# Optimization experiments

Measured on AMD Instinct MI355X. Metric: run time of the kernel, lower is better.

The kernel has to match this reference:

```python
import jax, jax.numpy as jnp
import numpy as np

POOL = 2  # maxout pool size


def setup_inputs() -> dict:
    key = jax.random.key(0)
    ks = jax.random.split(key, 20)
    V, WV, ENC, DEC, ATT = 32000, 512, 512, 512, 512
    T, B, S, L = 32, 64, 256, 1
    IN = WV + ENC  # input_feed: emb concat context
    sc = 0.02
    emb_table = jax.random.normal(ks[0], (V, WV), jnp.float32) * sc
    emb_table = emb_table.at[0].set(0.0)  # padding_idx = PAD = 0
    inp = {
        'input_ids': jax.random.randint(ks[1], (T, B), 0, V),
        'hidden': jax.random.normal(ks[2], (L, B, DEC), jnp.float32),
        'context': jax.random.normal(ks[3], (S, B, ENC), jnp.float32),
        'src_pad_mask': jnp.zeros((B, S), jnp.float32),
        'init_att': jax.random.normal(ks[4], (B, ENC), jnp.float32),
        'emb_table': emb_table,
        'W_ih': jax.random.normal(ks[5], (3 * DEC, IN), jnp.float32) * sc,
        'W_hh': jax.random.normal(ks[6], (3 * DEC, DEC), jnp.float32) * sc,
        'b_ih': jnp.zeros((3 * DEC,), jnp.float32),
        'b_hh': jnp.zeros((3 * DEC,), jnp.float32),
        'W_pre': jax.random.normal(ks[7], (ATT, ENC), jnp.float32) * sc,
        'b_pre': jnp.zeros((ATT,), jnp.float32),
        'W_q': jax.random.normal(ks[8], (ATT, DEC), jnp.float32) * sc,
        'v_att': jax.random.normal(ks[9], (ATT,), jnp.float32) * sc,
        'W_copy': jax.random.normal(ks[10], (1, ENC + DEC), jnp.float32) * sc,
        'b_copy': jnp.zeros((1,), jnp.float32),
        'W_read': jax.random.normal(ks[11], (DEC, ENC + DEC + WV), jnp.float32) * sc,
        'b_read': jnp.zeros((DEC,), jnp.float32),
    }
    return inp


def reference(input_ids, hidden, context, src_pad_mask, init_att, emb_table,
              W_ih, W_hh, b_ih, b_hh, W_pre, b_pre, W_q, v_att,
              W_copy, b_copy, W_read, b_read):
    T, B = input_ids.shape
    dec = hidden.shape[-1]
    ctx_t = jnp.transpose(context, (1, 0, 2))            # [B, S, enc]
    # ConcatAttention precompute (done once, reused each step)
    precompute = jnp.einsum('bse,ae->bsa', ctx_t, W_pre) + b_pre  # [B, S, att]
    emb = emb_table[input_ids]                           # [T, B, wv]

    def gru_cell(x, h):
        gx = x @ W_ih.T + b_ih
        gh = h @ W_hh.T + b_hh
        xr, xz, xn = jnp.split(gx, 3, axis=-1)
        hr, hz, hn = jnp.split(gh, 3, axis=-1)
        r = jax.nn.sigmoid(xr + hr)
        z = jax.nn.sigmoid(xz + hz)
        n = jnp.tanh(xn + r * hn)
        return (1.0 - z) * n + z * h

    def step(carry, emb_t):
        h, cur_ctx = carry                               # h: [1,B,dec]
        x = jnp.concatenate([emb_t, cur_ctx], axis=1)    # input_feed
        h_new = gru_cell(x, h[0])
        out = h_new                                      # single layer output
        # concat attention
        target = out @ W_q.T                             # [B, att]
        tmp = jnp.tanh(precompute + target[:, None, :])  # [B, S, att]
        energy = jnp.einsum('bsa,a->bs', tmp, v_att)
        energy = energy * (1.0 - src_pad_mask) + src_pad_mask * (-1e6)
        score = jax.nn.softmax(energy, axis=-1)          # [B, S]
        new_ctx = jnp.einsum('bs,bse->be', score, ctx_t)
        # copy gate
        copy_p = jax.nn.sigmoid(
            jnp.concatenate([out, new_ctx], axis=1) @ W_copy.T + b_copy)
        # readout + maxout (dropout is identity at eval)
        readout = jnp.concatenate([emb_t, out, new_ctx], axis=1) @ W_read.T + b_read
        mo = readout.reshape(B, dec // POOL, POOL).max(axis=-1)
        return (h_new[None], new_ctx), (mo, score, copy_p)

    (hid, cur_ctx), (g_out, c_out, copy_out) = jax.lax.scan(
        step, (hidden, init_att), emb)
    return g_out, c_out, copy_out, hid, c_out[-1], cur_ctx
```

## Files before the change

kernel.cpp:

```cpp
#include <hip/hip_runtime.h>
#include <hip/hip_bf16.h>


typedef unsigned int uint;
typedef unsigned short ushort;
typedef __attribute__((ext_vector_type(8))) short s8v;
typedef __attribute__((ext_vector_type(4))) float f4v;

#define DD 512

__device__ __forceinline__ float sigmf(float x) { return 1.0f / (1.0f + __expf(-x)); }
__device__ __forceinline__ float tanh_fast(float x) {
    float e = __expf(2.0f * x);
    return 1.0f - 2.0f / (e + 1.0f);
}
__device__ __forceinline__ ushort f2bf(float f) {
    uint b = __float_as_uint(f);
    return (ushort)((b + 0x7FFFu + ((b >> 16) & 1u)) >> 16);
}
__device__ __forceinline__ uint pk2(float a, float b) {
    return (uint)f2bf(a) | ((uint)f2bf(b) << 16);
}
__device__ __forceinline__ float bfl(uint u) { return __uint_as_float(u << 16); }
__device__ __forceinline__ float bfh(uint u) { return __uint_as_float(u & 0xFFFF0000u); }
__device__ __forceinline__ f4v MFMA(s8v a, s8v b, f4v c) {
    return __builtin_amdgcn_mfma_f32_16x16x32_bf16(a, b, c, 0, 0, 0);
}

__device__ __forceinline__ void gbar(uint* c, uint target) {
    __syncthreads();
    if (threadIdx.x == 0) {
        asm volatile("s_waitcnt vmcnt(0) lgkmcnt(0)" ::: "memory");
        __hip_atomic_fetch_add(c, 1u, __ATOMIC_RELAXED, __HIP_MEMORY_SCOPE_AGENT);
        while (__hip_atomic_load(c, __ATOMIC_RELAXED, __HIP_MEMORY_SCOPE_AGENT) < target)
            __builtin_amdgcn_s_sleep(1);
    }
    __syncthreads();
}

template <int MODE>
__global__ __launch_bounds__(256) void mgemm(
    const float* __restrict__ A0, const float* __restrict__ A1,
    const float* __restrict__ A2, const int* __restrict__ ids,
    const float* __restrict__ Bm, const float* __restrict__ bias,
    void* __restrict__ Cout, int ldb, int K)
{
    __shared__ __align__(16) ushort Ab[64 * 32];
    __shared__ __align__(16) ushort Bb[64 * 32];
    __shared__ int rid[64];
    const int tid = threadIdx.x;
    const int m0 = blockIdx.x * 64, n0 = blockIdx.y * 64;
    if (MODE != 0 && tid < 64) rid[tid] = ids[m0 + tid];
    const int lane = tid & 63;
    const int w = tid >> 6;
    const int srow = tid >> 2, sc = tid & 3;
    f4v acc[4];
#pragma unroll
    for (int mt = 0; mt < 4; ++mt) acc[mt] = (f4v){0.f, 0.f, 0.f, 0.f};

    for (int k0 = 0; k0 < K; k0 += 32) {
        __syncthreads();
        {
            const float* ap;
            int m = m0 + srow;
            if (MODE == 0) {
                ap = A0 + (size_t)(m & 255) * 32768 + (size_t)(m >> 8) * 512 + k0 + sc * 8;
            } else if (MODE == 1) {
                ap = A0 + (size_t)rid[srow] * 512 + k0 + sc * 8;
            } else {
                if (k0 < 512)       ap = A0 + (size_t)rid[srow] * 512 + k0 + sc * 8;
                else if (k0 < 1024) ap = A1 + (size_t)m * 512 + (k0 - 512) + sc * 8;
                else                ap = A2 + (size_t)m * 512 + (k0 - 1024) + sc * 8;
            }
            float4 v0 = *(const float4*)ap;
            float4 v1 = *(const float4*)(ap + 4);
            uint4 pa;
            pa.x = pk2(v0.x, v0.y); pa.y = pk2(v0.z, v0.w);
            pa.z = pk2(v1.x, v1.y); pa.w = pk2(v1.z, v1.w);
            *(uint4*)&Ab[srow * 32 + ((sc ^ (srow & 3)) << 3)] = pa;
            const float* bp = Bm + (size_t)(n0 + srow) * ldb + k0 + sc * 8;
            float4 w0 = *(const float4*)bp;
            float4 w1 = *(const float4*)(bp + 4);
            uint4 pb;
            pb.x = pk2(w0.x, w0.y); pb.y = pk2(w0.z, w0.w);
            pb.z = pk2(w1.x, w1.y); pb.w = pk2(w1.z, w1.w);
            *(uint4*)&Bb[srow * 32 + ((sc ^ (srow & 3)) << 3)] = pb;
        }
        __syncthreads();
        int rr = lane & 15, kc = lane >> 4;
        s8v bf = *(const s8v*)&Bb[(w * 16 + rr) * 32 + ((kc ^ (rr & 3)) << 3)];
#pragma unroll
        for (int mt = 0; mt < 4; ++mt) {
            s8v af = *(const s8v*)&Ab[(mt * 16 + rr) * 32 + ((kc ^ (rr & 3)) << 3)];
            acc[mt] = MFMA(af, bf, acc[mt]);
        }
    }
    float bv = bias[n0 + w * 16 + (lane & 15)];
#pragma unroll
    for (int mt = 0; mt < 4; ++mt) {
#pragma unroll
        for (int r2 = 0; r2 < 4; ++r2) {
            int m = m0 + mt * 16 + (lane >> 4) * 4 + r2;
            int n = n0 + w * 16 + (lane & 15);
            float v = acc[mt][r2] + bv;
            if (MODE == 0) {
                ((ushort*)Cout)[(size_t)m * 512 + n] = f2bf(v);
            } else if (MODE == 1) {
                ((float*)Cout)[(size_t)m * 1536 + n] = v;
            } else {
                float vm = fmaxf(v, __shfl_xor(v, 1));
                if (!(lane & 1)) ((float*)Cout)[(size_t)m * 256 + (n >> 1)] = vm;
            }
        }
    }
}

__global__ __launch_bounds__(512) void wprep2(
    const float* __restrict__ W_ih, const float* __restrict__ W_hh,
    const float* __restrict__ W_q,
    uint* __restrict__ Wpk, uint* __restrict__ WqT)
{
    int id = blockIdx.x * 512 + threadIdx.x;
    if (id < 786432) {
        int l4 = id & 255;
        int chunk = id >> 8;
        int g = chunk % 3;
        int t2 = chunk / 3;
        int ks = t2 & 15;
        int mat = (t2 >> 4) & 1;
        int u = t2 >> 5;
        int lane = l4 >> 2, e2 = l4 & 3;
        int n = g * 512 + u * 16 + (lane & 15);
        int k = ks * 32 + ((lane >> 4) << 3) + e2 * 2;
        float w0, w1;
        if (mat == 0) {
            w0 = W_ih[(size_t)n * 1024 + 512 + k];
            w1 = W_ih[(size_t)n * 1024 + 512 + k + 1];
        } else {
            w0 = W_hh[(size_t)n * 512 + k];
            w1 = W_hh[(size_t)n * 512 + k + 1];
        }
        Wpk[id] = pk2(w0, w1);
    } else if (id < 917504) {
        int rid2 = id - 786432;
        int kp = rid2 >> 9, a = rid2 & 511;
        WqT[rid2] = pk2(W_q[(size_t)a * 512 + 2 * kp], W_q[(size_t)a * 512 + 2 * kp + 1]);
    }
}

__global__ __launch_bounds__(512, 1) void k_steps(
    const float* __restrict__ gxe, const float* __restrict__ hidden,
    const float* __restrict__ init_att, const float* __restrict__ context,
    const float* __restrict__ mask, const float* __restrict__ v_att,
    const float* __restrict__ b_hh, const ushort* __restrict__ preb,
    const uint* __restrict__ Wpk, const uint* __restrict__ WqT,
    float* __restrict__ h_hist, float* __restrict__ ctx_hist,
    float* __restrict__ pe_buf, uint* __restrict__ cnt,
    float* __restrict__ cout)
{
    __shared__ __align__(16) ushort preT[256 * 128];
    __shared__ __align__(16) ushort ctxT[256 * 128];
    __shared__ __align__(16) float scr[6144];
    __shared__ float smask[256];
    __shared__ float svatt[128];

    const int tid = threadIdx.x;
    const int blk = blockIdx.x;
    const int q = blk >> 6;
    const int b = blk & 63;
    const int r = b & 7;
    const int u = ((b >> 3) << 2) | q;
    const int lane = tid & 63;
    const int wid = __builtin_amdgcn_readfirstlane(tid >> 6);

    uint* cl_cnt = cnt + b * 32;
    uint* gr_cnt = cnt + 2048 + r * 32;

#pragma unroll
    for (int cc = 0; cc < 8; ++cc) {
        int cid = tid * 8 + cc;
        int s = cid >> 4, ch = cid & 15;
        int sw = (s ^ (s >> 3)) & 7;
        uint4 pv = *(const uint4*)(preb + ((size_t)(b * 256 + s)) * 512 + q * 128 + ch * 8);
        *(uint4*)&preT[s * 128 + ((ch ^ sw) << 3)] = pv;
        const float* cp = context + ((size_t)s * 64 + b) * 512 + q * 128 + ch * 8;
        float4 c0 = *(const float4*)cp;
        float4 c1 = *(const float4*)(cp + 4);
        uint4 cv;
        cv.x = pk2(c0.x, c0.y); cv.y = pk2(c0.z, c0.w);
        cv.z = pk2(c1.x, c1.y); cv.w = pk2(c1.z, c1.w);
        *(uint4*)&ctxT[s * 128 + ch * 8] = cv;
    }
    if (tid < 256) smask[tid] = mask[b * 256 + tid];
    else if (tid < 384) svatt[tid - 256] = v_att[q * 128 + (tid - 256)];

    const int mat_w = wid >> 2, kw = wid & 3;
    s8v wr0[4], wr1[4], wr2[4];
#pragma unroll
    for (int s = 0; s < 4; ++s) {
        int ks = kw * 4 + s;
        const uint* wb = Wpk + ((((u * 2 + mat_w) * 16 + ks) * 3) << 8) + (lane << 2);
        wr0[s] = *(const s8v*)(wb);
        wr1[s] = *(const s8v*)(wb + 256);
        wr2[s] = *(const s8v*)(wb + 512);
    }
    const int a_p2 = tid & 127, dq_p2 = tid >> 7;
    uint wqreg[64];
#pragma unroll
    for (int i = 0; i < 64; ++i)
        wqreg[i] = WqT[(size_t)(dq_p2 * 64 + i) * 512 + q * 128 + a_p2];

    const int bloc = tid >> 4, jj = tid & 15;
    int bb_c = 0, d_c = 0, eidx = 0;
    float bh0 = 0.f, bh1 = 0.f, bh2 = 0.f;
    if (tid < 128) {
        bb_c = r + bloc * 8;
        d_c = u * 16 + jj;
        eidx = ((jj + ((bloc >> 2) << 4)) << 2) + (bloc & 3);
        bh0 = b_hh[d_c]; bh1 = b_hh[512 + d_c]; bh2 = b_hh[1024 + d_c];
    }

    for (int t = 0; t < 32; ++t) {
        const float* ctxp = t ? (ctx_hist + (size_t)(t - 1) * 32768) : init_att;
        const float* hp = t ? (h_hist + (size_t)(t - 1) * 32768) : hidden;

        float gx0 = 0.f, gx1 = 0.f, gx2 = 0.f, hpv = 0.f;
        if (tid < 128) {
            const float* gp = gxe + ((size_t)t * 64 + bb_c) * 1536 + d_c;
            gx0 = gp[0]; gx1 = gp[512]; gx2 = gp[1024];
            hpv = hp[(size_t)bb_c * 512 + d_c];
        }

        __syncthreads();
        {
            int c2 = tid & 31, row = (tid >> 5) & 7, mat = tid >> 8;
            const float* src = mat ? hp : ctxp;
            int bb = r + row * 8;
            const float* sp = src + (size_t)bb * 512 + c2 * 16;
            float4 v0 = *(const float4*)sp, v1 = *(const float4*)(sp + 4);
            float4 v2 = *(const float4*)(sp + 8), v3 = *(const float4*)(sp + 12);
            uint4 p0, p1;
            p0.x = pk2(v0.x, v0.y); p0.y = pk2(v0.z, v0.w);
            p0.z = pk2(v1.x, v1.y); p0.w = pk2(v1.z, v1.w);
            p1.x = pk2(v2.x, v2.y); p1.y = pk2(v2.z, v2.w);
            p1.z = pk2(v3.x, v3.y); p1.w = pk2(v3.z, v3.w);
            char* xb = (char*)scr + mat * 8192 + row * 1024;
            int c0 = c2 * 2;
            *(uint4*)(xb + ((c0 ^ row) << 4)) = p0;
            *(uint4*)(xb + (((c0 + 1) ^ row) << 4)) = p1;
        }
        __syncthreads();
        f4v ac0 = (f4v){0.f, 0.f, 0.f, 0.f};
        f4v ac1 = ac0, ac2 = ac0;
        {
            const char* xbase = (const char*)scr + mat_w * 8192 + (lane & 15) * 1024;
            int rsw = (lane & 15) & 7;
#pragma unroll
            for (int s = 0; s < 4; ++s) {
                int ch = kw * 16 + s * 4 + (lane >> 4);
                s8v af = *(const s8v*)(xbase + ((ch ^ rsw) << 4));
                ac0 = MFMA(af, wr0[s], ac0);
                ac1 = MFMA(af, wr1[s], ac1);
                ac2 = MFMA(af, wr2[s], ac2);
            }
        }
        __syncthreads();
        {
            f4v* rb = (f4v*)scr;
            rb[((mat_w * 3 + 0) * 4 + kw) * 64 + lane] = ac0;
            rb[((mat_w * 3 + 1) * 4 + kw) * 64 + lane] = ac1;
            rb[((mat_w * 3 + 2) * 4 + kw) * 64 + lane] = ac2;
        }
        __syncthreads();
        if (tid < 128) {
            float AX[3], AH[3];
#pragma unroll
            for (int g = 0; g < 3; ++g) {
                float sx = 0.f, sh = 0.f;
#pragma unroll
                for (int kw2 = 0; kw2 < 4; ++kw2) {
                    sx += scr[((0 + g) * 4 + kw2) * 256 + eidx];
                    sh += scr[((3 + g) * 4 + kw2) * 256 + eidx];
                }
                AX[g] = sx;
                AH[g] = sh;
            }
            AX[0] += gx0; AX[1] += gx1; AX[2] += gx2;
            AH[0] += bh0; AH[1] += bh1; AH[2] += bh2;
            float rr = sigmf(AX[0] + AH[0]);
            float zz = sigmf(AX[1] + AH[1]);
            float nn = tanh_fast(AX[2] + rr * AH[2]);
            h_hist[(size_t)t * 32768 + (size_t)bb_c * 512 + d_c] =
                (1.0f - zz) * nn + zz * hpv;
        }
        gbar(gr_cnt, (uint)(64 * t + 32));

        scr[tid] = h_hist[(size_t)t * 32768 + (size_t)b * 512 + tid];
        __syncthreads();
        {
            float acc = 0.f;
#pragma unroll
            for (int i = 0; i < 64; ++i) {
                uint w = wqreg[i];
                acc = fmaf(bfl(w), scr[(dq_p2 * 64 + i) * 2 + 0],
                           fmaf(bfh(w), scr[(dq_p2 * 64 + i) * 2 + 1], acc));
            }
            scr[512 + tid] = acc;
        }
        __syncthreads();
        if (tid < 128)
            scr[1024 + tid] = scr[512 + tid] + scr[640 + tid] +
                              scr[768 + tid] + scr[896 + tid];
        __syncthreads();

        {
            int s = tid & 255, hf = tid >> 8;
            int sw = (s ^ (s >> 3)) & 7;
            float acc = 0.f;
#pragma unroll
            for (int c8 = 0; c8 < 8; ++c8) {
                int ch = hf * 8 + c8;
                uint4 pv = *(const uint4*)&preT[s * 128 + ((ch ^ sw) << 3)];
                int ab = ch * 8;
                acc += svatt[ab + 0] * tanh_fast(bfl(pv.x) + scr[1024 + ab + 0]);
                acc += svatt[ab + 1] * tanh_fast(bfh(pv.x) + scr[1024 + ab + 1]);
                acc += svatt[ab + 2] * tanh_fast(bfl(pv.y) + scr[1024 + ab + 2]);
                acc += svatt[ab + 3] * tanh_fast(bfh(pv.y) + scr[1024 + ab + 3]);
                acc += svatt[ab + 4] * tanh_fast(bfl(pv.z) + scr[1024 + ab + 4]);
                acc += svatt[ab + 5] * tanh_fast(bfh(pv.z) + scr[1024 + ab + 5]);
                acc += svatt[ab + 6] * tanh_fast(bfl(pv.w) + scr[1024 + ab + 6]);
                acc += svatt[ab + 7] * tanh_fast(bfh(pv.w) + scr[1024 + ab + 7]);
            }
            scr[1280 + tid] = acc;
        }
        __syncthreads();
        if (tid < 256)
            pe_buf[((size_t)t * 64 + b) * 1024 + q * 256 + tid] =
                scr[1280 + tid] + scr[1536 + tid];
        gbar(cl_cnt, (uint)(4 * t + 4));

        {
            int s2 = tid & 255;
            const float* peb = pe_buf + ((size_t)t * 64 + b) * 1024;
            float e = peb[s2] + peb[256 + s2] + peb[512 + s2] + peb[768 + s2];
            float mk = smask[s2];
            e = e * (1.0f - mk) + mk * (-1e6f);
            float mx = e;
#pragma unroll
            for (int off = 1; off < 64; off <<= 1) mx = fmaxf(mx, __shfl_xor(mx, off));
            if (lane == 0) scr[2560 + wid] = mx;
            __syncthreads();
            mx = scr[2560];
#pragma unroll
            for (int w2 = 1; w2 < 8; ++w2) mx = fmaxf(mx, scr[2560 + w2]);
            float ex = __expf(e - mx);
            float sm = ex;
#pragma unroll
            for (int off = 1; off < 64; off <<= 1) sm += __shfl_xor(sm, off);
            if (lane == 0) scr[2568 + wid] = sm;
            __syncthreads();
            sm = scr[2568] + scr[2569] + scr[2570] + scr[2571];
            float sc = ex / sm;
            scr[1792 + s2] = sc;
            if (q == 0 && tid < 256) cout[((size_t)t * 64 + b) * 256 + tid] = sc;
        }
        __syncthreads();
        {
            int e_l = tid & 127, sq = tid >> 7;
            float acc = 0.f;
#pragma unroll 8
            for (int i = 0; i < 64; ++i) {
                int ss = sq * 64 + i;
                float cv = __uint_as_float(((uint)ctxT[ss * 128 + e_l]) << 16);
                acc = fmaf(scr[1792 + ss], cv, acc);
            }
            scr[2048 + tid] = acc;
        }
        __syncthreads();
        if (tid < 128) {
            float val = scr[2048 + tid] + scr[2176 + tid] +
                        scr[2304 + tid] + scr[2432 + tid];
            ctx_hist[(size_t)t * 32768 + (size_t)b * 512 + q * 128 + tid] = val;
        }
        gbar(gr_cnt, (uint)(64 * t + 64));
    }
}

__global__ __launch_bounds__(256) void k_copy(
    const float* __restrict__ h_hist, const float* __restrict__ ctx_hist,
    const float* __restrict__ W_copy, const float* __restrict__ b_copy,
    float* __restrict__ out)
{
    const int tid = threadIdx.x;
    const int lane = tid & 63;
    const int tb = blockIdx.x * 4 + (tid >> 6);
    const float* hp = h_hist + (size_t)tb * DD;
    const float* cp = ctx_hist + (size_t)tb * DD;
    float acc = 0.f;
#pragma unroll
    for (int jj = 0; jj < 8; ++jj) {
        int k = lane + 64 * jj;
        acc = fmaf(hp[k], W_copy[k], acc);
        acc = fmaf(cp[k], W_copy[512 + k], acc);
    }
#pragma unroll
    for (int off = 1; off < 64; off <<= 1) acc += __shfl_xor(acc, off);
    if (lane == 0) out[tb] = sigmf(acc + b_copy[0]);
}

__global__ void k_final(const float* __restrict__ h_hist,
                        const float* __restrict__ ctx_hist,
                        float* __restrict__ dout)
{
    int idx = blockIdx.x * 256 + threadIdx.x;
    if (idx < 32768) {
        dout[1050624 + idx] = h_hist[31 * 32768 + idx];
    } else if (idx < 49152) {
        int i2 = idx - 32768;
        dout[1083392 + i2] = dout[524288 + 507904 + i2];
    } else {
        int i2 = idx - 49152;
        dout[1099776 + i2] = ctx_hist[31 * 32768 + i2];
    }
}

extern "C" void kernel_launch(void* const* d_in, const int* in_sizes, int n_in,
                              void* d_out, int out_size, void* d_ws, size_t ws_size,
                              hipStream_t stream)
{
    (void)in_sizes; (void)n_in; (void)out_size; (void)ws_size;
    const int*   ids      = (const int*)d_in[0];
    const float* hidden   = (const float*)d_in[1];
    const float* context  = (const float*)d_in[2];
    const float* mask     = (const float*)d_in[3];
    const float* init_att = (const float*)d_in[4];
    const float* emb_t    = (const float*)d_in[5];
    const float* W_ih     = (const float*)d_in[6];
    const float* W_hh     = (const float*)d_in[7];
    const float* b_ih     = (const float*)d_in[8];
    const float* b_hh     = (const float*)d_in[9];
    const float* W_pre    = (const float*)d_in[10];
    const float* b_pre    = (const float*)d_in[11];
    const float* W_q      = (const float*)d_in[12];
    const float* v_att    = (const float*)d_in[13];
    const float* W_copy   = (const float*)d_in[14];
    const float* b_copy   = (const float*)d_in[15];
    const float* W_read   = (const float*)d_in[16];
    const float* b_read   = (const float*)d_in[17];
    float* out = (float*)d_out;
    float* ws = (float*)d_ws;

    ushort* preb    = (ushort*)ws;
    float* gxe      = ws + 4194304;
    float* h_hist   = ws + 7340032;
    float* ctx_hist = ws + 8388608;
    float* pe_buf   = ws + 9437184;
    uint* Wpk       = (uint*)(ws + 11534336);
    uint* WqT       = (uint*)(ws + 12320768);
    uint* cnt       = (uint*)(ws + 12451840);
    float* cout     = out + 524288;

    hipMemsetAsync(cnt, 0, 16384, stream);
    mgemm<0><<<dim3(256, 8), 256, 0, stream>>>(context, nullptr, nullptr, nullptr,
                                               W_pre, b_pre, (void*)preb, 512, 512);
    mgemm<1><<<dim3(32, 24), 256, 0, stream>>>(emb_t, nullptr, nullptr, ids,
                                               W_ih, b_ih, (void*)gxe, 1024, 512);
    wprep2<<<1792, 512, 0, stream>>>(W_ih, W_hh, W_q, Wpk, WqT);
    {
        void* args[] = {
            (void*)&gxe, (void*)&hidden, (void*)&init_att, (void*)&context,
            (void*)&mask, (void*)&v_att, (void*)&b_hh, (void*)&preb,
            (void*)&Wpk, (void*)&WqT,
            (void*)&h_hist, (void*)&ctx_hist, (void*)&pe_buf, (void*)&cnt,
            (void*)&cout
        };
        hipLaunchCooperativeKernel((void*)k_steps, dim3(256), dim3(512), args, 0,
                                   stream);
    }
    mgemm<2><<<dim3(32, 8), 256, 0, stream>>>(emb_t, h_hist, ctx_hist, ids,
                                              W_read, b_read, (void*)out, 1536, 1536);
    k_copy<<<512, 256, 0, stream>>>(h_hist, ctx_hist, W_copy, b_copy, out + 1048576);
    k_final<<<320, 256, 0, stream>>>(h_hist, ctx_hist, out);
}
```

Measured before the change: 641.9 us.

## Replace atomic-counter grid barriers with per-member flag arrays and leader release

Replaces the fetch-add counter barrier with a flag-based barrier. Each member block stores a tag in its own slot, the leader block polls all slots in parallel across threads and then writes a release flag that the other members spin on. This is meant to cut contention on a single atomic counter and to remove the sleep-based polling latency across the many sequential timesteps. It also reworks the context-weighted sum so each thread handles two bf16 elements over 32 sources with an 8-way reduction. The busy spin without sleep may add memory traffic while blocks wait.

After: 643.4 us. Within noise of the previous version (+0.2%).

```diff
diff --git a/kernel.cpp b/kernel.cpp
--- a/kernel.cpp
+++ b/kernel.cpp
@@ -27,13 +27,28 @@
     return __builtin_amdgcn_mfma_f32_16x16x32_bf16(a, b, c, 0, 0, 0);
 }
 
-__device__ __forceinline__ void gbar(uint* c, uint target) {
+__device__ __forceinline__ void flag_bar(uint* arr, uint* rel, int member,
+                                         int nmem, uint tag) {
     __syncthreads();
-    if (threadIdx.x == 0) {
+    const int tid = threadIdx.x;
+    if (tid == 0) {
         asm volatile("s_waitcnt vmcnt(0) lgkmcnt(0)" ::: "memory");
-        __hip_atomic_fetch_add(c, 1u, __ATOMIC_RELAXED, __HIP_MEMORY_SCOPE_AGENT);
-        while (__hip_atomic_load(c, __ATOMIC_RELAXED, __HIP_MEMORY_SCOPE_AGENT) < target)
-            __builtin_amdgcn_s_sleep(1);
+        __hip_atomic_store(arr + member, tag, __ATOMIC_RELAXED,
+                           __HIP_MEMORY_SCOPE_AGENT);
+    }
+    if (member == 0) {
+        if (tid > 0 && tid < nmem) {
+            while (__hip_atomic_load(arr + tid, __ATOMIC_RELAXED,
+                                     __HIP_MEMORY_SCOPE_AGENT) < tag) {}
+        }
+        if (tid == 0)
+            __hip_atomic_store(rel, tag, __ATOMIC_RELAXED,
+                               __HIP_MEMORY_SCOPE_AGENT);
+    } else {
+        if (tid == 0) {
+            while (__hip_atomic_load(rel, __ATOMIC_RELAXED,
+                                     __HIP_MEMORY_SCOPE_AGENT) < tag) {}
+        }
     }
     __syncthreads();
 }
@@ -173,8 +188,10 @@
     const int lane = tid & 63;
     const int wid = __builtin_amdgcn_readfirstlane(tid >> 6);
 
-    uint* cl_cnt = cnt + b * 32;
-    uint* gr_cnt = cnt + 2048 + r * 32;
+    uint* garr = cnt + r * 64;
+    uint* grel = cnt + 512 + r * 16;
+    uint* carr = cnt + 1024 + b * 8;
+    uint* crel = cnt + 2048 + b * 16;
 
 #pragma unroll
     for (int cc = 0; cc < 8; ++cc) {
@@ -293,7 +310,7 @@
             h_hist[(size_t)t * 32768 + (size_t)bb_c * 512 + d_c] =
                 (1.0f - zz) * nn + zz * hpv;
         }
-        gbar(gr_cnt, (uint)(64 * t + 32));
+        flag_bar(garr, grel, u, 32, (uint)(t * 4 + 1));
 
         scr[tid] = h_hist[(size_t)t * 32768 + (size_t)b * 512 + tid];
         __syncthreads();
@@ -337,7 +354,7 @@
         if (tid < 256)
             pe_buf[((size_t)t * 64 + b) * 1024 + q * 256 + tid] =
                 scr[1280 + tid] + scr[1536 + tid];
-        gbar(cl_cnt, (uint)(4 * t + 4));
+        flag_bar(carr, crel, q, 4, (uint)(t * 4 + 2));
 
         {
             int s2 = tid & 255;
@@ -348,41 +365,45 @@
             float mx = e;
 #pragma unroll
             for (int off = 1; off < 64; off <<= 1) mx = fmaxf(mx, __shfl_xor(mx, off));
-            if (lane == 0) scr[2560 + wid] = mx;
+            if (lane == 0) scr[3072 + wid] = mx;
             __syncthreads();
-            mx = scr[2560];
-#pragma unroll
-            for (int w2 = 1; w2 < 8; ++w2) mx = fmaxf(mx, scr[2560 + w2]);
+            mx = scr[3072];
+#pragma unroll
+            for (int w2 = 1; w2 < 8; ++w2) mx = fmaxf(mx, scr[3072 + w2]);
             float ex = __expf(e - mx);
             float sm = ex;
 #pragma unroll
             for (int off = 1; off < 64; off <<= 1) sm += __shfl_xor(sm, off);
-            if (lane == 0) scr[2568 + wid] = sm;
+            if (lane == 0) scr[3080 + wid] = sm;
             __syncthreads();
-            sm = scr[2568] + scr[2569] + scr[2570] + scr[2571];
+            sm = scr[3080] + scr[3081] + scr[3082] + scr[3083];
             float sc = ex / sm;
             scr[1792 + s2] = sc;
             if (q == 0 && tid < 256) cout[((size_t)t * 64 + b) * 256 + tid] = sc;
         }
         __syncthreads();
         {
-            int e_l = tid & 127, sq = tid >> 7;
-            float acc = 0.f;
+            int e2 = tid & 63, sq = tid >> 6;
+            float acc0 = 0.f, acc1 = 0.f;
 #pragma unroll 8
-            for (int i = 0; i < 64; ++i) {
-                int ss = sq * 64 + i;
-                float cv = __uint_as_float(((uint)ctxT[ss * 128 + e_l]) << 16);
-                acc = fmaf(scr[1792 + ss], cv, acc);
-            }
-            scr[2048 + tid] = acc;
+            for (int i = 0; i < 32; ++i) {
+                int ss = sq * 32 + i;
+                uint cv = *(const uint*)&ctxT[ss * 128 + e2 * 2];
+                float sc = scr[1792 + ss];
+                acc0 = fmaf(sc, bfl(cv), acc0);
+                acc1 = fmaf(sc, bfh(cv), acc1);
+            }
+            scr[2048 + sq * 128 + e2 * 2 + 0] = acc0;
+            scr[2048 + sq * 128 + e2 * 2 + 1] = acc1;
         }
         __syncthreads();
         if (tid < 128) {
-            float val = scr[2048 + tid] + scr[2176 + tid] +
-                        scr[2304 + tid] + scr[2432 + tid];
+            float val = 0.f;
+#pragma unroll
+            for (int s8 = 0; s8 < 8; ++s8) val += scr[2048 + s8 * 128 + tid];
             ctx_hist[(size_t)t * 32768 + (size_t)b * 512 + q * 128 + tid] = val;
         }
-        gbar(gr_cnt, (uint)(64 * t + 64));
+        flag_bar(garr, grel, u, 32, (uint)(t * 4 + 3));
     }
 }
 
```
